# Kernel tuning notes

Hardware: AMD Instinct MI355X
Metric: run time of the kernel (lower is better)

Reference implementation:

```python
import jax, jax.numpy as jnp
import numpy as np

H = 256
W = 256
N_BLOCKS = 3  # default n_blocks in CBModel


def _scatter_heatmap_sample0(coords, B, C):
    """Faithful to original loop: uses coords from batch index 0 for ALL j in range(B)
    (the source indexes gen_pose{1,2}_cor[0, i, :] regardless of j).
    coords: [C, 2] float. Returns [B, C, H, W]."""
    x = jnp.trunc(coords[:, 0]).astype(jnp.int32)  # int() truncates toward zero
    y = jnp.trunc(coords[:, 1]).astype(jnp.int32)
    valid = (x >= 0) & (x <= 255) & (y >= 0) & (y <= 255)
    xc = jnp.clip(x, 0, 255)
    yc = jnp.clip(y, 0, 255)
    # each keypoint writes into its own channel -> clipped-invalid writes of 0 are no-ops
    hm = jnp.zeros((C, H, W), coords.dtype).at[jnp.arange(C), xc, yc].set(valid.astype(coords.dtype))
    return jnp.broadcast_to(hm[None], (B, C, H, W))


def _scatter_heatmap_batched(coords):
    """coords: [B, C, 2] float -> [B, C, H, W] one-hot heatmaps (per-sample coords,
    matching the inner step_pose double loop over i in B, j in C)."""
    B, C, _ = coords.shape
    x = jnp.trunc(coords[..., 0]).astype(jnp.int32)
    y = jnp.trunc(coords[..., 1]).astype(jnp.int32)
    valid = (x >= 0) & (x <= 255) & (y >= 0) & (y <= 255)
    xc = jnp.clip(x, 0, 255)
    yc = jnp.clip(y, 0, 255)
    bb = jnp.arange(B)[:, None]
    cc = jnp.arange(C)[None, :]
    return jnp.zeros((B, C, H, W), coords.dtype).at[bb, cc, xc, yc].set(valid.astype(coords.dtype))


def setup_inputs() -> dict:
    key = jax.random.key(0)
    k1, k2 = jax.random.split(key)
    B, C = 32, 18
    # coordinates roughly in-frame, some slightly out of [0,255] to exercise bounds check
    pose1_cor = jax.random.uniform(k1, (B, C, 2), jnp.float32, -8.0, 264.0)
    pose2_cor = jax.random.uniform(k2, (B, C, 2), jnp.float32, -8.0, 264.0)
    return {"pose1_cor": pose1_cor, "pose2_cor": pose2_cor}


def reference(pose1_cor, pose2_cor):
    B, C, _ = pose1_cor.shape
    # gen_poses[0/1]: heatmaps scattered from sample-0 coords, replicated over batch
    gp0 = _scatter_heatmap_sample0(pose1_cor[0], B, C)
    gp1 = _scatter_heatmap_sample0(pose2_cor[0], B, C)
    gen_poses = jnp.stack([gp0, gp1], axis=0)  # [2, B, C, H, W]

    # step = (gen_pose2_cor - gen_pose1_cor) // n_blocks  (floor division on floats)
    step = jnp.floor_divide(pose2_cor - pose1_cor, jnp.float32(N_BLOCKS))
    step_pose_cor = pose1_cor
    step_heatmaps = []
    for _ in range(N_BLOCKS - 1):  # intermediate blocks scatter interpolated poses
        step_pose_cor = step_pose_cor + step
        step_heatmaps.append(_scatter_heatmap_batched(step_pose_cor))
    step_poses = jnp.stack(step_heatmaps, axis=0)  # [n_blocks-1, B, C, H, W]
    return gen_poses, step_poses
```

## Files before the change

### kernel.cpp

```cpp
#include <hip/hip_runtime.h>

#define HH 256
#define WW 256
#define HWSZ (HH * WW)
#define BB 32
#define CC 18
#define NBLK 3

__global__ void scatter_points(const float* __restrict__ pose1,
                               const float* __restrict__ pose2,
                               float* __restrict__ out) {
    int idx = blockIdx.x * blockDim.x + threadIdx.x;
    if (idx >= BB * CC) return;
    const int b = idx / CC;
    const int c = idx % CC;

    {
        const float xf = pose1[(size_t)c * 2 + 0];
        const float yf = pose1[(size_t)c * 2 + 1];
        const int x = (int)truncf(xf);
        const int y = (int)truncf(yf);
        if (x >= 0 && x <= 255 && y >= 0 && y <= 255) {
            out[((size_t)(0 * BB + b) * CC + c) * HWSZ + (size_t)x * WW + y] = 1.0f;
        }
    }
    {
        const float xf = pose2[(size_t)c * 2 + 0];
        const float yf = pose2[(size_t)c * 2 + 1];
        const int x = (int)truncf(xf);
        const int y = (int)truncf(yf);
        if (x >= 0 && x <= 255 && y >= 0 && y <= 255) {
            out[((size_t)(1 * BB + b) * CC + c) * HWSZ + (size_t)x * WW + y] = 1.0f;
        }
    }

    const float p1x = pose1[(size_t)idx * 2 + 0];
    const float p1y = pose1[(size_t)idx * 2 + 1];
    const float p2x = pose2[(size_t)idx * 2 + 0];
    const float p2y = pose2[(size_t)idx * 2 + 1];
    const float sx = floorf((p2x - p1x) / (float)NBLK);
    const float sy = floorf((p2y - p1y) / (float)NBLK);

    float cx = p1x + sx;
    float cy = p1y + sy;
    const size_t step_base = (size_t)2 * BB * CC * HWSZ;
    #pragma unroll
    for (int k = 0; k < NBLK - 1; ++k) {
        const int x = (int)truncf(cx);
        const int y = (int)truncf(cy);
        if (x >= 0 && x <= 255 && y >= 0 && y <= 255) {
            out[step_base + ((size_t)(k * BB + b) * CC + c) * HWSZ + (size_t)x * WW + y] = 1.0f;
        }
        cx += sx;
        cy += sy;
    }
}

extern "C" void kernel_launch(void* const* d_in, const int* in_sizes, int n_in,
                              void* d_out, int out_size, void* d_ws, size_t ws_size,
                              hipStream_t stream) {
    const float* pose1 = (const float*)d_in[0];
    const float* pose2 = (const float*)d_in[1];
    float* out = (float*)d_out;

    hipMemsetAsync(d_out, 0, (size_t)out_size * sizeof(float), stream);

    const int npts = BB * CC;
    scatter_points<<<(npts + 255) / 256, 256, 0, stream>>>(pose1, pose2, out);
}
```

Measured before the change: 568.3 us.

## Fuse zero-fill and point scatter into one per-plane kernel

Replaces the separate memset plus scatter launch with one kernel that has one block per output plane. Each block zeroes its 256x256 plane with vectorized float4 stores, then the thread that wrote the float4 holding the target pixel sets it to 1.0. Because that thread rewrites its own earlier store, no barrier is needed. This removes a launch and the ordering between memset and scatter, at the cost of relying on the kernel's store bandwidth matching the driver memset for about 150 MB of writes.

```diff
diff --git a/kernel.cpp b/kernel.cpp
--- a/kernel.cpp
+++ b/kernel.cpp
@@ -6,53 +6,53 @@
 #define BB 32
 #define CC 18
 #define NBLK 3
+#define NPLANES (4 * BB * CC)
 
-__global__ void scatter_points(const float* __restrict__ pose1,
-                               const float* __restrict__ pose2,
-                               float* __restrict__ out) {
-    int idx = blockIdx.x * blockDim.x + threadIdx.x;
-    if (idx >= BB * CC) return;
-    const int b = idx / CC;
-    const int c = idx % CC;
+typedef float v4f __attribute__((ext_vector_type(4)));
 
-    {
-        const float xf = pose1[(size_t)c * 2 + 0];
-        const float yf = pose1[(size_t)c * 2 + 1];
-        const int x = (int)truncf(xf);
-        const int y = (int)truncf(yf);
-        if (x >= 0 && x <= 255 && y >= 0 && y <= 255) {
-            out[((size_t)(0 * BB + b) * CC + c) * HWSZ + (size_t)x * WW + y] = 1.0f;
-        }
+__global__ void __launch_bounds__(256)
+fill_scatter(const float* __restrict__ pose1,
+             const float* __restrict__ pose2,
+             float* __restrict__ out) {
+    const int plane = blockIdx.x;
+    const int outer = plane / (BB * CC);
+    const int rem   = plane % (BB * CC);
+    const int c     = rem % CC;
+
+    float xf, yf;
+    if (outer == 0) {
+        xf = pose1[(size_t)c * 2 + 0];
+        yf = pose1[(size_t)c * 2 + 1];
+    } else if (outer == 1) {
+        xf = pose2[(size_t)c * 2 + 0];
+        yf = pose2[(size_t)c * 2 + 1];
+    } else {
+        const float p1x = pose1[(size_t)rem * 2 + 0];
+        const float p1y = pose1[(size_t)rem * 2 + 1];
+        const float p2x = pose2[(size_t)rem * 2 + 0];
+        const float p2y = pose2[(size_t)rem * 2 + 1];
+        const float sx = floorf((p2x - p1x) / (float)NBLK);
+        const float sy = floorf((p2y - p1y) / (float)NBLK);
+        xf = p1x + sx;
+        yf = p1y + sy;
+        if (outer == 3) { xf += sx; yf += sy; }
     }
-    {
-        const float xf = pose2[(size_t)c * 2 + 0];
-        const float yf = pose2[(size_t)c * 2 + 1];
-        const int x = (int)truncf(xf);
-        const int y = (int)truncf(yf);
-        if (x >= 0 && x <= 255 && y >= 0 && y <= 255) {
-            out[((size_t)(1 * BB + b) * CC + c) * HWSZ + (size_t)x * WW + y] = 1.0f;
-        }
+    const int x = (int)truncf(xf);
+    const int y = (int)truncf(yf);
+    const bool valid = (x >= 0 && x <= 255 && y >= 0 && y <= 255);
+    const int tgt = valid ? (x * WW + y) : -1;
+
+    float* plane_base = out + (size_t)plane * HWSZ;
+    v4f* p4 = (v4f*)plane_base;
+    const v4f z = (v4f)(0.f);
+    const int t = threadIdx.x;
+    #pragma unroll
+    for (int k = 0; k < 64; ++k) {
+        p4[k * 256 + t] = z;
     }
 
-    const float p1x = pose1[(size_t)idx * 2 + 0];
-    const float p1y = pose1[(size_t)idx * 2 + 1];
-    const float p2x = pose2[(size_t)idx * 2 + 0];
-    const float p2y = pose2[(size_t)idx * 2 + 1];
-    const float sx = floorf((p2x - p1x) / (float)NBLK);
-    const float sy = floorf((p2y - p1y) / (float)NBLK);
-
-    float cx = p1x + sx;
-    float cy = p1y + sy;
-    const size_t step_base = (size_t)2 * BB * CC * HWSZ;
-    #pragma unroll
-    for (int k = 0; k < NBLK - 1; ++k) {
-        const int x = (int)truncf(cx);
-        const int y = (int)truncf(cy);
-        if (x >= 0 && x <= 255 && y >= 0 && y <= 255) {
-            out[step_base + ((size_t)(k * BB + b) * CC + c) * HWSZ + (size_t)x * WW + y] = 1.0f;
-        }
-        cx += sx;
-        cy += sy;
+    if (tgt >= 0 && t == ((tgt >> 2) & 255)) {
+        plane_base[tgt] = 1.0f;
     }
 }
 
@@ -63,8 +63,5 @@
     const float* pose2 = (const float*)d_in[1];
     float* out = (float*)d_out;
 
-    hipMemsetAsync(d_out, 0, (size_t)out_size * sizeof(float), stream);
-
-    const int npts = BB * CC;
-    scatter_points<<<(npts + 255) / 256, 256, 0, stream>>>(pose1, pose2, out);
+    fill_scatter<<<NPLANES, 256, 0, stream>>>(pose1, pose2, out);
 }
```

Result: slower. 580.2 us (+2.1%).
